# Optimization experiments

Hardware: AMD Instinct MI355X
Metric: run time of the kernel (lower is better)

## Reference

```python
import jax, jax.numpy as jnp
import numpy as np

VOCAB = 198
DEPTH = 512
NPAIR = (DEPTH - 1) // 2  # 255: columns 510,511 left as zero (matches original loop bound)


def _positional_matrix(seq_len):
    i = jnp.arange(seq_len, dtype=jnp.float32)[:, None]          # [L,1]
    j = jnp.arange(NPAIR, dtype=jnp.float32)[None, :]            # [1,255]
    angle = i / jnp.power(10000.0, 2.0 * j / DEPTH)              # [L,255]
    pe = jnp.zeros((seq_len, DEPTH), dtype=jnp.float32)
    pe = pe.at[:, 0:2 * NPAIR:2].set(jnp.sin(angle))
    pe = pe.at[:, 1:2 * NPAIR:2].set(jnp.cos(angle))
    return pe


def setup_inputs() -> dict:
    key = jax.random.key(0)
    k1, k2 = jax.random.split(key)
    idx = jax.random.randint(k1, (131072,), 0, VOCAB, dtype=jnp.int32)
    wordlist = jax.random.normal(k2, (VOCAB, DEPTH), dtype=jnp.float32)
    return {"idx": idx, "wordlist": wordlist}


def reference(idx, wordlist):
    # gather token embeddings: [L, DEPTH]
    emb = wordlist[idx]
    pe = _positional_matrix(idx.shape[0])
    return emb + pe
```

## Files before the change

### kernel.cpp

```cpp
#include <hip/hip_runtime.h>


#define L_TOTAL 131072
#define VEC_PER_ROW 128
#define R 32
#define CHUNK 8

typedef float f32x4 __attribute__((ext_vector_type(4)));
typedef int   i32x4 __attribute__((ext_vector_type(4)));

__device__ __forceinline__ void sincos_fast(float a, float& s, float& c) {
    const float INV2PI = 0.15915493667125702f;
    const float PI2_HI = 6.2831854820251465f;
    const float PI2_LO = -1.7484555314695172e-7f;
    float k = rintf(a * INV2PI);
    float r = fmaf(-k, PI2_HI, a);
    r = fmaf(-k, PI2_LO, r);
    float rev = r * INV2PI;
    s = __builtin_amdgcn_sinf(rev);
    c = __builtin_amdgcn_cosf(rev);
}

__global__ __launch_bounds__(256) void embed_pe_kernel(
    const int* __restrict__ idx,
    const float* __restrict__ wordlist,
    float* __restrict__ out)
{
    int t  = blockIdx.x * 256 + threadIdx.x;
    int rb = t >> 7;
    int cc = t & 127;
    int i0 = rb * R;

    const float K = 0.051905126483205076f;
    float invf0 = exp2f(-(float)(2 * cc)     * K);
    float invf1 = exp2f(-(float)(2 * cc + 1) * K);

    float s0, c0, s1, c1, sd0, cd0, sd1, cd1;
    sincos_fast((float)i0 * invf0, s0, c0);
    sincos_fast((float)i0 * invf1, s1, c1);
    sincos_fast(invf0, sd0, cd0);
    sincos_fast(invf1, sd1, cd1);

    if (cc == VEC_PER_ROW - 1) { s1 = 0.0f; c1 = 0.0f; }

    const i32x4* ip = (const i32x4*)idx + rb * (R / 4);
    const f32x4* wl = (const f32x4*)wordlist;
    f32x4*       op = (f32x4*)out + (size_t)i0 * VEC_PER_ROW + cc;

#pragma unroll
    for (int ch = 0; ch < R / CHUNK; ++ch) {
        i32x4 ta = ip[ch * 2];
        i32x4 tb = ip[ch * 2 + 1];
        int tok[CHUNK] = { ta[0], ta[1], ta[2], ta[3],
                           tb[0], tb[1], tb[2], tb[3] };

#pragma unroll
        for (int k = 0; k < CHUNK; ++k) {
            f32x4 w = wl[tok[k] * VEC_PER_ROW + cc];
            f32x4 o;
            o[0] = w[0] + s0;
            o[1] = w[1] + c0;
            o[2] = w[2] + s1;
            o[3] = w[3] + c1;
            op[(size_t)(ch * CHUNK + k) * VEC_PER_ROW] = o;

            float ns0 = fmaf(s0, cd0, c0 * sd0);
            float nc0 = fmaf(c0, cd0, -s0 * sd0);
            s0 = ns0; c0 = nc0;
            float ns1 = fmaf(s1, cd1, c1 * sd1);
            float nc1 = fmaf(c1, cd1, -s1 * sd1);
            s1 = ns1; c1 = nc1;
        }
    }
}

extern "C" void kernel_launch(void* const* d_in, const int* in_sizes, int n_in,
                              void* d_out, int out_size, void* d_ws, size_t ws_size,
                              hipStream_t stream) {
    const int*   idx      = (const int*)d_in[0];
    const float* wordlist = (const float*)d_in[1];
    float*       out      = (float*)d_out;

    int total_threads = (L_TOTAL / R) * VEC_PER_ROW;
    int block = 256;
    int grid = total_threads / block;
    embed_pe_kernel<<<grid, block, 0, stream>>>(idx, wordlist, out);
}
```

Before: 254.9 us.

## Stage wordlist column slice in LDS and split blocks by column chunk

Each block now loads a 128-byte column slice of all 198 vocab rows into shared memory, with an XOR swizzle to avoid bank conflicts. It then gathers token embeddings from LDS instead of global memory. The thread mapping changes so each block covers one column chunk for 32 row groups. Each wave now writes only 128 contiguous bytes per row, which may hurt store coalescing, and every block adds the cost of loading the table slice plus a barrier.

```diff
diff --git a/kernel.cpp b/kernel.cpp
--- a/kernel.cpp
+++ b/kernel.cpp
@@ -2,9 +2,12 @@
 
 
 #define L_TOTAL 131072
-#define VEC_PER_ROW 128
+#define DEPTH_F4 128
 #define R 32
-#define CHUNK 8
+#define CCQ 8
+#define NCHUNK 16
+#define RG_PER_BLOCK 32
+#define VOCAB 198
 
 typedef float f32x4 __attribute__((ext_vector_type(4)));
 typedef int   i32x4 __attribute__((ext_vector_type(4)));
@@ -26,10 +29,27 @@
     const float* __restrict__ wordlist,
     float* __restrict__ out)
 {
-    int t  = blockIdx.x * 256 + threadIdx.x;
-    int rb = t >> 7;
-    int cc = t & 127;
-    int i0 = rb * R;
+    __shared__ f32x4 lds[VOCAB * CCQ];
+
+    int tid   = threadIdx.x;
+    int bid   = blockIdx.x;
+    int chunk = bid >> 7;
+    int rgb   = bid & 127;
+
+    for (int u = tid; u < VOCAB * CCQ; u += 256) {
+        int r = u >> 3, g = u & 7;
+        f32x4 v = ((const f32x4*)wordlist)[r * DEPTH_F4 + chunk * CCQ + g];
+        lds[r * CCQ + (g ^ (r & 7))] = v;
+    }
+    __syncthreads();
+
+    int wave = tid >> 6;
+    int lane = tid & 63;
+    int rgl  = lane >> 3;
+    int ccq  = lane & 7;
+    int rg   = rgb * RG_PER_BLOCK + wave * 8 + rgl;
+    int i0   = rg * R;
+    int cc   = chunk * CCQ + ccq;
 
     const float K = 0.051905126483205076f;
     float invf0 = exp2f(-(float)(2 * cc)     * K);
@@ -41,28 +61,28 @@
     sincos_fast(invf0, sd0, cd0);
     sincos_fast(invf1, sd1, cd1);
 
-    if (cc == VEC_PER_ROW - 1) { s1 = 0.0f; c1 = 0.0f; }
+    if (cc == DEPTH_F4 - 1) { s1 = 0.0f; c1 = 0.0f; }
 
-    const i32x4* ip = (const i32x4*)idx + rb * (R / 4);
-    const f32x4* wl = (const f32x4*)wordlist;
-    f32x4*       op = (f32x4*)out + (size_t)i0 * VEC_PER_ROW + cc;
+    const i32x4* ip = (const i32x4*)idx + rg * (R / 4);
+    f32x4*       op = (f32x4*)out + (size_t)i0 * DEPTH_F4 + cc;
 
 #pragma unroll
-    for (int ch = 0; ch < R / CHUNK; ++ch) {
+    for (int ch = 0; ch < R / 8; ++ch) {
         i32x4 ta = ip[ch * 2];
         i32x4 tb = ip[ch * 2 + 1];
-        int tok[CHUNK] = { ta[0], ta[1], ta[2], ta[3],
-                           tb[0], tb[1], tb[2], tb[3] };
+        int tok[8] = { ta[0], ta[1], ta[2], ta[3],
+                       tb[0], tb[1], tb[2], tb[3] };
 
 #pragma unroll
-        for (int k = 0; k < CHUNK; ++k) {
-            f32x4 w = wl[tok[k] * VEC_PER_ROW + cc];
+        for (int k = 0; k < 8; ++k) {
+            int t = tok[k];
+            f32x4 w = lds[t * CCQ + (ccq ^ (t & 7))];
             f32x4 o;
             o[0] = w[0] + s0;
             o[1] = w[1] + c0;
             o[2] = w[2] + s1;
             o[3] = w[3] + c1;
-            op[(size_t)(ch * CHUNK + k) * VEC_PER_ROW] = o;
+            op[(size_t)(ch * 8 + k) * DEPTH_F4] = o;
 
             float ns0 = fmaf(s0, cd0, c0 * sd0);
             float nc0 = fmaf(c0, cd0, -s0 * sd0);
@@ -81,8 +101,6 @@
     const float* wordlist = (const float*)d_in[1];
     float*       out      = (float*)d_out;
 
-    int total_threads = (L_TOTAL / R) * VEC_PER_ROW;
-    int block = 256;
-    int grid = total_threads / block;
-    embed_pe_kernel<<<grid, block, 0, stream>>>(idx, wordlist, out);
+    int grid = (L_TOTAL / R / RG_PER_BLOCK) * NCHUNK;
+    embed_pe_kernel<<<grid, 256, 0, stream>>>(idx, wordlist, out);
 }
```

Result: no change. 259.5 us (+1.8%).

## Restructure into wave-per-row-strip blocks with token indices staged in LDS

Applied to the files above, without the earlier changes.

Each block now covers 512 rows and each 64-lane wave owns a 128-row strip, with every lane handling two float4 columns of a row. Token indices are first loaded into LDS and then read per chunk, and gathers are batched four rows at a time. The goal is fewer per-thread sincos setups relative to the rows written, and coalesced index loads. The cost is a grid of only 256 blocks (one per CU, four waves each), which cuts occupancy and memory-level parallelism. The longer angle-addition recurrence across 128 rows also lets rounding drift accumulate.

```diff
diff --git a/kernel.cpp b/kernel.cpp
--- a/kernel.cpp
+++ b/kernel.cpp
@@ -2,12 +2,11 @@
 
 
 #define L_TOTAL 131072
-#define VEC_PER_ROW 128
-#define R 32
-#define CHUNK 8
+#define ROWS_PER_BLOCK 512
+#define ROWS_PER_WAVE 128
+#define CHUNK 4
 
 typedef float f32x4 __attribute__((ext_vector_type(4)));
-typedef int   i32x4 __attribute__((ext_vector_type(4)));
 
 __device__ __forceinline__ void sincos_fast(float a, float& s, float& c) {
     const float INV2PI = 0.15915493667125702f;
@@ -26,50 +25,81 @@
     const float* __restrict__ wordlist,
     float* __restrict__ out)
 {
-    int t  = blockIdx.x * 256 + threadIdx.x;
-    int rb = t >> 7;
-    int cc = t & 127;
-    int i0 = rb * R;
+    __shared__ int idx_lds[ROWS_PER_BLOCK];
+
+    int tid     = threadIdx.x;
+    int bid     = blockIdx.x;
+    int rowbase = bid * ROWS_PER_BLOCK;
+
+    for (int u = tid; u < ROWS_PER_BLOCK; u += 256)
+        idx_lds[u] = idx[rowbase + u];
+    __syncthreads();
+
+    int wave  = tid >> 6;
+    int lane  = tid & 63;
+    int wrow0 = wave * ROWS_PER_WAVE;
+    int i0    = rowbase + wrow0;
 
     const float K = 0.051905126483205076f;
-    float invf0 = exp2f(-(float)(2 * cc)     * K);
-    float invf1 = exp2f(-(float)(2 * cc + 1) * K);
+    float invf0 = exp2f(-(float)(2 * lane)       * K);
+    float invf1 = exp2f(-(float)(2 * lane + 1)   * K);
+    float invf2 = exp2f(-(float)(2 * lane + 128) * K);
+    float invf3 = exp2f(-(float)(2 * lane + 129) * K);
 
-    float s0, c0, s1, c1, sd0, cd0, sd1, cd1;
+    float s0, c0, s1, c1, s2, c2, s3, c3;
+    float sd0, cd0, sd1, cd1, sd2, cd2, sd3, cd3;
     sincos_fast((float)i0 * invf0, s0, c0);
     sincos_fast((float)i0 * invf1, s1, c1);
+    sincos_fast((float)i0 * invf2, s2, c2);
+    sincos_fast((float)i0 * invf3, s3, c3);
     sincos_fast(invf0, sd0, cd0);
     sincos_fast(invf1, sd1, cd1);
+    sincos_fast(invf2, sd2, cd2);
+    sincos_fast(invf3, sd3, cd3);
 
-    if (cc == VEC_PER_ROW - 1) { s1 = 0.0f; c1 = 0.0f; }
+    if (lane == 63) { s3 = 0.0f; c3 = 0.0f; }
 
-    const i32x4* ip = (const i32x4*)idx + rb * (R / 4);
     const f32x4* wl = (const f32x4*)wordlist;
-    f32x4*       op = (f32x4*)out + (size_t)i0 * VEC_PER_ROW + cc;
+    f32x4*       op = (f32x4*)out + (size_t)i0 * 128 + lane;
 
+    for (int ch = 0; ch < ROWS_PER_WAVE / CHUNK; ++ch) {
+        int toks[CHUNK];
 #pragma unroll
-    for (int ch = 0; ch < R / CHUNK; ++ch) {
-        i32x4 ta = ip[ch * 2];
-        i32x4 tb = ip[ch * 2 + 1];
-        int tok[CHUNK] = { ta[0], ta[1], ta[2], ta[3],
-                           tb[0], tb[1], tb[2], tb[3] };
+        for (int k = 0; k < CHUNK; ++k)
+            toks[k] = idx_lds[wrow0 + ch * CHUNK + k];
+
+        f32x4 wa[CHUNK], wb[CHUNK];
+#pragma unroll
+        for (int k = 0; k < CHUNK; ++k) {
+            const f32x4* p = wl + (size_t)toks[k] * 128 + lane;
+            wa[k] = p[0];
+            wb[k] = p[64];
+        }
 
 #pragma unroll
         for (int k = 0; k < CHUNK; ++k) {
-            f32x4 w = wl[tok[k] * VEC_PER_ROW + cc];
-            f32x4 o;
-            o[0] = w[0] + s0;
-            o[1] = w[1] + c0;
-            o[2] = w[2] + s1;
-            o[3] = w[3] + c1;
-            op[(size_t)(ch * CHUNK + k) * VEC_PER_ROW] = o;
+            int r = ch * CHUNK + k;
+            f32x4 o0, o1;
+            o0[0] = wa[k][0] + s0;
+            o0[1] = wa[k][1] + c0;
+            o0[2] = wa[k][2] + s1;
+            o0[3] = wa[k][3] + c1;
+            o1[0] = wb[k][0] + s2;
+            o1[1] = wb[k][1] + c2;
+            o1[2] = wb[k][2] + s3;
+            o1[3] = wb[k][3] + c3;
+            op[(size_t)r * 128]      = o0;
+            op[(size_t)r * 128 + 64] = o1;
 
-            float ns0 = fmaf(s0, cd0, c0 * sd0);
-            float nc0 = fmaf(c0, cd0, -s0 * sd0);
-            s0 = ns0; c0 = nc0;
-            float ns1 = fmaf(s1, cd1, c1 * sd1);
-            float nc1 = fmaf(c1, cd1, -s1 * sd1);
-            s1 = ns1; c1 = nc1;
+            float t;
+            t  = fmaf(s0, cd0, c0 * sd0);
+            c0 = fmaf(c0, cd0, -s0 * sd0); s0 = t;
+            t  = fmaf(s1, cd1, c1 * sd1);
+            c1 = fmaf(c1, cd1, -s1 * sd1); s1 = t;
+            t  = fmaf(s2, cd2, c2 * sd2);
+            c2 = fmaf(c2, cd2, -s2 * sd2); s2 = t;
+            t  = fmaf(s3, cd3, c3 * sd3);
+            c3 = fmaf(c3, cd3, -s3 * sd3); s3 = t;
         }
     }
 }
@@ -81,8 +111,6 @@
     const float* wordlist = (const float*)d_in[1];
     float*       out      = (float*)d_out;
 
-    int total_threads = (L_TOTAL / R) * VEC_PER_ROW;
-    int block = 256;
-    int grid = total_threads / block;
-    embed_pe_kernel<<<grid, block, 0, stream>>>(idx, wordlist, out);
+    int grid = L_TOTAL / ROWS_PER_BLOCK;
+    embed_pe_kernel<<<grid, 256, 0, stream>>>(idx, wordlist, out);
 }
```

Result: no change. 259.3 us (+1.7%).
